# Optimization experiments

Hardware: AMD Instinct MI355X
Metric: run time of the kernel (lower is better)

The kernel has to match this reference:

```python
import jax, jax.numpy as jnp
import numpy as np

B, LMAX, M, D, V = 32768, 24, 10, 300, 36  # batch, max word len, max_length, embedding_dim, vocab


def setup_inputs() -> dict:
    key = jax.random.key(0)
    k1, k2, k3, k4 = jax.random.split(key, 4)
    lengths = jax.random.randint(k2, (B,), 1, LMAX + 1)  # word lengths in [1, LMAX]
    tokens = jax.random.randint(k1, (B, LMAX), 0, V)
    # zero out slots past each word's length (they are never read with nonzero weight)
    tokens = jnp.where(jnp.arange(LMAX)[None, :] < lengths[:, None], tokens, 0)
    emb_table = jax.random.normal(k3, (V, D), dtype=jnp.float32)
    pad_table = jax.random.normal(k4, (1, D), dtype=jnp.float32)
    return {"emb_table": emb_table, "pad_table": pad_table,
            "tokens": tokens, "lengths": lengths}


def reference(emb_table, pad_table, tokens, lengths):
    # Per-word char embedding lookup: [B, LMAX, D]
    embs = emb_table[tokens]

    # ---- interpolate branch (words with L >= M): bilinear, align_corners=True.
    # Output width == input width (D) so width interp is identity; only the
    # character axis is linearly resampled: src = i * (L-1) / (M-1).
    Lf = lengths.astype(jnp.float32)[:, None]                      # [B,1]
    pos = jnp.arange(M, dtype=jnp.float32)[None, :] * (Lf - 1.0) / (M - 1)  # [B,M]
    lo = jnp.floor(pos).astype(jnp.int32)                          # [B,M]
    hi = jnp.minimum(lo + 1, lengths[:, None].astype(jnp.int32) - 1)
    w = (pos - lo.astype(jnp.float32))[..., None]                  # [B,M,1]
    g_lo = jnp.take_along_axis(embs, lo[..., None], axis=1)        # [B,M,D]
    g_hi = jnp.take_along_axis(embs, hi[..., None], axis=1)        # [B,M,D]
    interp = g_lo * (1.0 - w) + g_hi * w

    # ---- padding branch (words with L < M): first L rows are embeddings,
    # remaining rows are the learned padding embedding.
    pad_vec = pad_table[0]                                         # [D]
    valid = jnp.arange(M)[None, :, None] < lengths[:, None, None]  # [B,M,1]
    padded = jnp.where(valid, embs[:, :M, :], pad_vec)

    out = jnp.where((lengths < M)[:, None, None], padded, interp)  # [B,M,D]
    return out
```

## Files before the change

### kernel.cpp

```cpp
#include <hip/hip_runtime.h>

#define BATCH 32768
#define LMAX  24
#define MOUT  10
#define DIM   300
#define VOCAB 36
#define D4    (DIM / 4)
#define N4    (BATCH * MOUT * D4)

__global__ __launch_bounds__(256) void word_emb_kernel(
    const float* __restrict__ emb,
    const float* __restrict__ pad,
    const int*   __restrict__ tokens,
    const int*   __restrict__ lengths,
    float4*      __restrict__ out)
{
    __shared__ float lds_emb[VOCAB * DIM];
    __shared__ float lds_pad[DIM];
    {
        const float4* emb4 = (const float4*)emb;
        float4* lemb4 = (float4*)lds_emb;
        for (int i = threadIdx.x; i < VOCAB * D4; i += blockDim.x)
            lemb4[i] = emb4[i];
        const float4* pad4 = (const float4*)pad;
        float4* lpad4 = (float4*)lds_pad;
        for (int i = threadIdx.x; i < D4; i += blockDim.x)
            lpad4[i] = pad4[i];
    }
    __syncthreads();

    const int stride = gridDim.x * blockDim.x;
    for (int e = blockIdx.x * blockDim.x + threadIdx.x; e < N4; e += stride) {
        const int row = e / D4;
        const int j   = e - row * D4;
        const int b   = row / MOUT;
        const int i   = row - b * MOUT;
        const int L   = lengths[b];

        float4 val;
        if (L < MOUT) {
            if (i < L) {
                const int tok = tokens[b * LMAX + i];
                val = *(const float4*)&lds_emb[tok * DIM + 4 * j];
            } else {
                val = *(const float4*)&lds_pad[4 * j];
            }
        } else {
            const float pos = (float)(i * (L - 1)) / (float)(MOUT - 1);
            const int   lo  = (int)floorf(pos);
            const int   hi  = min(lo + 1, L - 1);
            const float w   = pos - (float)lo;
            const int tlo = tokens[b * LMAX + lo];
            const int thi = tokens[b * LMAX + hi];
            const float4 glo = *(const float4*)&lds_emb[tlo * DIM + 4 * j];
            const float4 ghi = *(const float4*)&lds_emb[thi * DIM + 4 * j];
            const float wl = 1.0f - w;
            val.x = glo.x * wl + ghi.x * w;
            val.y = glo.y * wl + ghi.y * w;
            val.z = glo.z * wl + ghi.z * w;
            val.w = glo.w * wl + ghi.w * w;
        }
        out[e] = val;
    }
}

extern "C" void kernel_launch(void* const* d_in, const int* in_sizes, int n_in,
                              void* d_out, int out_size, void* d_ws, size_t ws_size,
                              hipStream_t stream) {
    const float* emb     = (const float*)d_in[0];
    const float* pad     = (const float*)d_in[1];
    const int*   tokens  = (const int*)d_in[2];
    const int*   lengths = (const int*)d_in[3];
    float4* out = (float4*)d_out;

    const int blocks = 768;
    word_emb_kernel<<<blocks, 256, 0, stream>>>(emb, pad, tokens, lengths, out);
}
```

Measured before the change: 465.5 us.

## Precompute per-row gather descriptors and run a branchless, unrolled fill kernel

A new pre-pass kernel computes, for every output row, the LDS offsets of the low and high source rows plus the interpolation weight, and writes them into the workspace as int4 descriptors. The main kernel then does a uniform weighted blend with no branches, using 512-thread blocks, a fixed grid that divides the work exactly, and a 4x unrolled loop. This removes repeated per-element length and token lookups and warp divergence, but adds a second launch and roughly 5 MB of descriptor traffic. A fallback keeps the old single-kernel path when the workspace is too small.

```diff
diff --git a/kernel.cpp b/kernel.cpp
--- a/kernel.cpp
+++ b/kernel.cpp
@@ -6,59 +6,146 @@
 #define DIM   300
 #define VOCAB 36
 #define D4    (DIM / 4)
-#define N4    (BATCH * MOUT * D4)
+#define NROW  (BATCH * MOUT)
+#define N4    (NROW * D4)
+#define PAD_OFF (VOCAB * DIM)
+#define LDSF  (VOCAB * DIM + DIM)
 
-__global__ __launch_bounds__(256) void word_emb_kernel(
+__global__ __launch_bounds__(256) void desc_kernel(
+    const int* __restrict__ lengths,
+    const int* __restrict__ tokens,
+    int4*      __restrict__ desc)
+{
+    const int r = blockIdx.x * blockDim.x + threadIdx.x;
+    if (r >= NROW) return;
+    const int b = r / MOUT;
+    const int i = r - b * MOUT;
+    const int L = lengths[b];
+
+    int lo_off, hi_off;
+    float w;
+    if (L < MOUT) {
+        if (i < L) {
+            lo_off = hi_off = tokens[b * LMAX + i] * DIM;
+        } else {
+            lo_off = hi_off = PAD_OFF;
+        }
+        w = 0.0f;
+    } else {
+        const float pos = ((float)i * (float)(L - 1)) / (float)(MOUT - 1);
+        const int   lo  = (int)floorf(pos);
+        const int   hi  = min(lo + 1, L - 1);
+        w = pos - (float)lo;
+        lo_off = tokens[b * LMAX + lo] * DIM;
+        hi_off = tokens[b * LMAX + hi] * DIM;
+    }
+    desc[r] = make_int4(lo_off, hi_off, __float_as_int(w), 0);
+}
+
+#define TPB   512
+#define NBLK  750
+#define NTHR  (TPB * NBLK)
+#define ITERS (N4 / NTHR)
+
+__global__ __launch_bounds__(TPB) void emb_kernel(
     const float* __restrict__ emb,
     const float* __restrict__ pad,
-    const int*   __restrict__ tokens,
-    const int*   __restrict__ lengths,
+    const int4*  __restrict__ desc,
     float4*      __restrict__ out)
 {
-    __shared__ float lds_emb[VOCAB * DIM];
-    __shared__ float lds_pad[DIM];
+    __shared__ float lds[LDSF];
     {
-        const float4* emb4 = (const float4*)emb;
-        float4* lemb4 = (float4*)lds_emb;
-        for (int i = threadIdx.x; i < VOCAB * D4; i += blockDim.x)
-            lemb4[i] = emb4[i];
-        const float4* pad4 = (const float4*)pad;
-        float4* lpad4 = (float4*)lds_pad;
-        for (int i = threadIdx.x; i < D4; i += blockDim.x)
-            lpad4[i] = pad4[i];
+        const float4* e4 = (const float4*)emb;
+        float4* l4 = (float4*)lds;
+        for (int i = threadIdx.x; i < VOCAB * D4; i += TPB) l4[i] = e4[i];
+        const float4* p4 = (const float4*)pad;
+        for (int i = threadIdx.x; i < D4; i += TPB) l4[VOCAB * D4 + i] = p4[i];
     }
     __syncthreads();
 
+    const int tid = blockIdx.x * TPB + threadIdx.x;
+    const int stride = NTHR;
+
+    int e = tid;
+    for (int it = 0; it < ITERS / 4; ++it) {
+        const int e0 = e, e1 = e + stride, e2 = e + 2 * stride, e3 = e + 3 * stride;
+
+        const int r0 = e0 / D4, r1 = e1 / D4, r2 = e2 / D4, r3 = e3 / D4;
+        const int j0 = e0 - r0 * D4, j1 = e1 - r1 * D4, j2 = e2 - r2 * D4, j3 = e3 - r3 * D4;
+
+        const int4 d0 = desc[r0];
+        const int4 d1 = desc[r1];
+        const int4 d2 = desc[r2];
+        const int4 d3 = desc[r3];
+
+        const float4 a0 = *(const float4*)&lds[d0.x + 4 * j0];
+        const float4 b0 = *(const float4*)&lds[d0.y + 4 * j0];
+        const float4 a1 = *(const float4*)&lds[d1.x + 4 * j1];
+        const float4 b1 = *(const float4*)&lds[d1.y + 4 * j1];
+        const float4 a2 = *(const float4*)&lds[d2.x + 4 * j2];
+        const float4 b2 = *(const float4*)&lds[d2.y + 4 * j2];
+        const float4 a3 = *(const float4*)&lds[d3.x + 4 * j3];
+        const float4 b3 = *(const float4*)&lds[d3.y + 4 * j3];
+
+        const float w0 = __int_as_float(d0.z), u0 = 1.0f - w0;
+        const float w1 = __int_as_float(d1.z), u1 = 1.0f - w1;
+        const float w2 = __int_as_float(d2.z), u2 = 1.0f - w2;
+        const float w3 = __int_as_float(d3.z), u3 = 1.0f - w3;
+
+        float4 v0, v1, v2, v3;
+        v0.x = a0.x * u0 + b0.x * w0; v0.y = a0.y * u0 + b0.y * w0;
+        v0.z = a0.z * u0 + b0.z * w0; v0.w = a0.w * u0 + b0.w * w0;
+        v1.x = a1.x * u1 + b1.x * w1; v1.y = a1.y * u1 + b1.y * w1;
+        v1.z = a1.z * u1 + b1.z * w1; v1.w = a1.w * u1 + b1.w * w1;
+        v2.x = a2.x * u2 + b2.x * w2; v2.y = a2.y * u2 + b2.y * w2;
+        v2.z = a2.z * u2 + b2.z * w2; v2.w = a2.w * u2 + b2.w * w2;
+        v3.x = a3.x * u3 + b3.x * w3; v3.y = a3.y * u3 + b3.y * w3;
+        v3.z = a3.z * u3 + b3.z * w3; v3.w = a3.w * u3 + b3.w * w3;
+
+        out[e0] = v0;
+        out[e1] = v1;
+        out[e2] = v2;
+        out[e3] = v3;
+
+        e += 4 * stride;
+    }
+}
+
+__global__ __launch_bounds__(256) void emb_kernel_fallback(
+    const float* __restrict__ emb, const float* __restrict__ pad,
+    const int* __restrict__ tokens, const int* __restrict__ lengths,
+    float4* __restrict__ out)
+{
+    __shared__ float lds[LDSF];
+    {
+        const float4* e4 = (const float4*)emb;
+        float4* l4 = (float4*)lds;
+        for (int i = threadIdx.x; i < VOCAB * D4; i += blockDim.x) l4[i] = e4[i];
+        const float4* p4 = (const float4*)pad;
+        for (int i = threadIdx.x; i < D4; i += blockDim.x) l4[VOCAB * D4 + i] = p4[i];
+    }
+    __syncthreads();
     const int stride = gridDim.x * blockDim.x;
     for (int e = blockIdx.x * blockDim.x + threadIdx.x; e < N4; e += stride) {
         const int row = e / D4;
-        const int j   = e - row * D4;
-        const int b   = row / MOUT;
-        const int i   = row - b * MOUT;
-        const int L   = lengths[b];
-
+        const int j = e - row * D4;
+        const int b = row / MOUT;
+        const int i = row - b * MOUT;
+        const int L = lengths[b];
         float4 val;
         if (L < MOUT) {
-            if (i < L) {
-                const int tok = tokens[b * LMAX + i];
-                val = *(const float4*)&lds_emb[tok * DIM + 4 * j];
-            } else {
-                val = *(const float4*)&lds_pad[4 * j];
-            }
+            val = (i < L) ? *(const float4*)&lds[tokens[b * LMAX + i] * DIM + 4 * j]
+                          : *(const float4*)&lds[PAD_OFF + 4 * j];
         } else {
-            const float pos = (float)(i * (L - 1)) / (float)(MOUT - 1);
-            const int   lo  = (int)floorf(pos);
-            const int   hi  = min(lo + 1, L - 1);
-            const float w   = pos - (float)lo;
-            const int tlo = tokens[b * LMAX + lo];
-            const int thi = tokens[b * LMAX + hi];
-            const float4 glo = *(const float4*)&lds_emb[tlo * DIM + 4 * j];
-            const float4 ghi = *(const float4*)&lds_emb[thi * DIM + 4 * j];
+            const float pos = ((float)i * (float)(L - 1)) / (float)(MOUT - 1);
+            const int lo = (int)floorf(pos);
+            const int hi = min(lo + 1, L - 1);
+            const float w = pos - (float)lo;
+            const float4 glo = *(const float4*)&lds[tokens[b * LMAX + lo] * DIM + 4 * j];
+            const float4 ghi = *(const float4*)&lds[tokens[b * LMAX + hi] * DIM + 4 * j];
             const float wl = 1.0f - w;
-            val.x = glo.x * wl + ghi.x * w;
-            val.y = glo.y * wl + ghi.y * w;
-            val.z = glo.z * wl + ghi.z * w;
-            val.w = glo.w * wl + ghi.w * w;
+            val.x = glo.x * wl + ghi.x * w; val.y = glo.y * wl + ghi.y * w;
+            val.z = glo.z * wl + ghi.z * w; val.w = glo.w * wl + ghi.w * w;
         }
         out[e] = val;
     }
@@ -73,6 +160,12 @@
     const int*   lengths = (const int*)d_in[3];
     float4* out = (float4*)d_out;
 
-    const int blocks = 768;
-    word_emb_kernel<<<blocks, 256, 0, stream>>>(emb, pad, tokens, lengths, out);
+    const size_t desc_bytes = (size_t)NROW * sizeof(int4);
+    if (ws_size >= desc_bytes) {
+        int4* desc = (int4*)d_ws;
+        desc_kernel<<<(NROW + 255) / 256, 256, 0, stream>>>(lengths, tokens, desc);
+        emb_kernel<<<NBLK, TPB, 0, stream>>>(emb, pad, desc, out);
+    } else {
+        emb_kernel_fallback<<<768, 256, 0, stream>>>(emb, pad, tokens, lengths, out);
+    }
 }
```

Result: faster. 402.9 us (-13.5%).
